# Optimization experiments

Measured on AMD Instinct MI355X. Metric: run time of the kernel, lower is better.

The kernel has to match this reference:

```python
import jax, jax.numpy as jnp
import numpy as np

DYN_CH = 16   # dyn_ch
MASK_CH = 16  # mask_ch (use_low_level_info=True -> num_bases=16)
UP_F = 8      # upsample_f
POUT = 256    # pad_out_channel


def _conv(x, w, padding):
    # NCHW conv, stride 1
    return jax.lax.conv_general_dilated(x, w, (1, 1), padding,
                                        dimension_numbers=('NCHW', 'OIHW', 'NCHW'))


def _bn(x, scale, shift):
    # inference-mode (Sync)BatchNorm folded to affine: scale=gamma/sqrt(var+eps), shift=beta-mean*scale
    return x * scale[None, :, None, None] + shift[None, :, None, None]


def _padconv(x, w, b, cin, cout, relu):
    # Faithful math of padconv(repeat -> mul -> grouped ones-conv -> bias -> relu),
    # expressed as a per-pixel dynamic 1x1 conv. Since w/b are nearest-upsampled
    # from HxW by factor f, we contract at low resolution per fxf block instead of
    # materializing the cout*cin-channel repeated tensors.
    # x: [B, cin, H*f, W*f]; w: [B, cout*cin, H, W]; b: [B, cout, H, W]
    B, _, Hf, Wf = x.shape
    H, W = w.shape[2], w.shape[3]
    f = Hf // H
    xb = x.reshape(B, cin, H, f, W, f)
    wr = w.reshape(B, cout, cin, H, W)
    out = jnp.einsum('bchpwq,bochw->bohpwq', xb, wr) + b[:, :, :, None, :, None]
    out = out.reshape(B, cout, Hf, Wf)
    return jax.nn.relu(out) if relu else out


def setup_inputs() -> dict:
    key = jax.random.key(0)
    ks = jax.random.split(key, 8)
    B, H, W = 8, 16, 16
    f = UP_F
    num_out = (2 + 16) * 16 + 16 + 16 * 16 + 16 + 16 * 256 + 256  # 4928
    inp = {}
    inp['res5'] = jax.random.normal(ks[0], (B, 2048, H, W), jnp.float32)
    inp['res2'] = jax.random.normal(ks[1], (B, 256, H * f, W * f), jnp.float32)
    inp['bottleneck_w'] = jax.random.normal(ks[2], (512, 2048, 3, 3), jnp.float32) * 0.01
    inp['bn1_scale'] = jnp.ones((512,), jnp.float32)
    inp['bn1_shift'] = jnp.zeros((512,), jnp.float32)
    inp['cls0_w'] = jax.random.normal(ks[3], (1024, 1024, 3, 3), jnp.float32) * 0.01
    inp['bn2_scale'] = jnp.ones((1024,), jnp.float32)
    inp['bn2_shift'] = jnp.zeros((1024,), jnp.float32)
    inp['cls1_w'] = jax.random.normal(ks[4], (num_out, 1024, 1, 1), jnp.float32) * 0.01
    inp['cls1_b'] = jnp.zeros((num_out,), jnp.float32)
    inp['c1a_w'] = jax.random.normal(ks[5], (48, 256, 3, 3), jnp.float32) * 0.02
    inp['bn3_scale'] = jnp.ones((48,), jnp.float32)
    inp['bn3_shift'] = jnp.zeros((48,), jnp.float32)
    inp['c1b_w'] = jax.random.normal(ks[6], (16, 48, 1, 1), jnp.float32) * 0.05
    inp['c1b_b'] = jnp.zeros((16,), jnp.float32)
    inp['cat_scale'] = jnp.ones((18,), jnp.float32)
    inp['cat_shift'] = jnp.zeros((18,), jnp.float32)
    return inp


def reference(res5, res2, bottleneck_w, bn1_scale, bn1_shift, cls0_w, bn2_scale,
              bn2_shift, cls1_w, cls1_b, c1a_w, bn3_scale, bn3_shift, c1b_w,
              c1b_b, cat_scale, cat_shift):
    B, _, H, W = res5.shape
    f = UP_F
    # bottleneck: conv3x3 -> BN -> relu
    x = jax.nn.relu(_bn(_conv(res5, bottleneck_w, 'SAME'), bn1_scale, bn1_shift))
    # global image pool, broadcast back, concat
    gp = jnp.broadcast_to(jnp.mean(x, axis=(2, 3), keepdims=True), x.shape)
    x = jnp.concatenate([x, gp], axis=1)
    # classifier: conv3x3 -> BN -> relu -> conv1x1 (+bias) => hyper-network params
    x = jax.nn.relu(_bn(_conv(x, cls0_w, 'SAME'), bn2_scale, bn2_shift))
    x = _conv(x, cls1_w, 'VALID') + cls1_b[None, :, None, None]  # [B, 4928, H, W]
    # c1_bottleneck on res2 (low-level features at H*f x W*f)
    c1 = jax.nn.relu(_bn(_conv(res2, c1a_w, 'SAME'), bn3_scale, bn3_shift))
    c1 = _conv(c1, c1b_w, 'VALID') + c1b_b[None, :, None, None]  # [B, 16, H*f, W*f]
    # split hyper-net output into per-pixel MLP weights/biases
    ch, nb = DYN_CH, MASK_CH
    sizes = [(2 + nb) * ch, ch, ch * ch, ch, ch * POUT, POUT]
    splits = np.cumsum(sizes)[:-1].tolist()
    w0, b0, w1, b1, w2, b2 = jnp.split(x, splits, axis=1)
    # coord grid: per fxf block, (x, y) in [0,1), tiled over HxW blocks
    xs = jnp.arange(f, dtype=jnp.float32) / f
    gy, gx = jnp.meshgrid(xs, xs, indexing='ij')
    loc = jnp.stack([gx, gy], axis=0)               # [2, f, f]
    coord = jnp.tile(loc, (1, H, W))                # [2, H*f, W*f]
    coord = jnp.broadcast_to(coord[None], (B, 2, H * f, W * f))
    inp = _bn(jnp.concatenate([coord, c1], axis=1), cat_scale, cat_shift)  # cat_norm
    # 3-layer per-pixel dynamic MLP (padconv trick, fused here)
    h = _padconv(inp, w0, b0, 2 + nb, ch, True)
    h = _padconv(h, w1, b1, ch, ch, True)
    out = _padconv(h, w2, b2, ch, POUT, False)      # [B, 256, H*f, W*f]
    return out
```

## Files before the change

### kernel.cpp

```cpp
#include <hip/hip_runtime.h>

#define B8 8

typedef __attribute__((ext_vector_type(8))) short short8;
typedef __attribute__((ext_vector_type(4))) float floatx4;

static __device__ __forceinline__ unsigned short f2bf(float f) {
  unsigned int u = __float_as_uint(f);
  unsigned int r = (u + 0x7fffu + ((u >> 16) & 1u)) >> 16;
  return (unsigned short)r;
}

__global__ __launch_bounds__(256) void wtransform(
    const float* __restrict__ w, unsigned short* __restrict__ wT,
    int Cout, int Cin)
{
  int idx = blockIdx.x * 256 + threadIdx.x;
  if (idx >= Cout * Cin) return;
  int ci = idx % Cin, co = idx / Cin;
  const float* s = w + (size_t)idx * 9;
#pragma unroll
  for (int t = 0; t < 9; ++t)
    wT[((size_t)t * Cout + co) * Cin + ci] = f2bf(s[t]);
}

__global__ __launch_bounds__(256) void cvt_bf16(
    const float* __restrict__ w, unsigned short* __restrict__ o, int n)
{
  int i = blockIdx.x * 256 + threadIdx.x;
  if (i < n) o[i] = f2bf(w[i]);
}

__global__ __launch_bounds__(256, 2) void conv3x3_mfma(
    const void* __restrict__ inv,
    const unsigned short* __restrict__ wT,
    float* __restrict__ part, int Cin, int Cout, int nCoBlk, int nSlice,
    int inBf16)
{
  int t = blockIdx.x;
  int slice = t % nSlice; t /= nSlice;
  int ph = t & 1; t >>= 1;
  int cb = t % nCoBlk; t /= nCoBlk;
  int b = t;
  int ciSlice = Cin / nSlice;
  int nTiles = ciSlice >> 5;

  __shared__ unsigned short sIn[10 * 18 * 40];

  int tid = threadIdx.x;
  int lane = tid & 63, wave = tid >> 6;
  int wc = wave >> 1, wp = wave & 1;
  int l15 = lane & 15, q = lane >> 4;

  for (int i = tid; i < (10 * 18 * 40) / 2; i += 256) ((unsigned int*)sIn)[i] = 0u;

  floatx4 acc[4][4];
#pragma unroll
  for (int ct = 0; ct < 4; ++ct)
#pragma unroll
    for (int pt = 0; pt < 4; ++pt) acc[ct][pt] = (floatx4){0.f, 0.f, 0.f, 0.f};

  int coBase = cb * 128 + wc * 64;
  int gr0 = ph * 7;
  int sr0 = 1 - ph;

  int gofs[18], lofs[18];
#pragma unroll
  for (int k = 0; k < 18; ++k) {
    int i = tid + k * 256;
    int px = i & 15, r9 = i >> 4;
    int rr = r9 % 9, ci = r9 / 9;
    gofs[k] = ci * 256 + (gr0 + rr) * 16 + px;
    lofs[k] = ((sr0 + rr) * 18 + 1 + px) * 40 + ci;
  }
  const float* inbF = (const float*)inv + (size_t)b * Cin * 256;
  const unsigned short* inbU = (const unsigned short*)inv + (size_t)b * Cin * 256;

  unsigned int pf[18];
  {
    int ci0 = slice * ciSlice;
    if (inBf16) {
#pragma unroll
      for (int k = 0; k < 18; ++k) pf[k] = inbU[(size_t)ci0 * 256 + gofs[k]];
    } else {
#pragma unroll
      for (int k = 0; k < 18; ++k)
        pf[k] = __float_as_uint(inbF[(size_t)ci0 * 256 + gofs[k]]);
    }
  }

  for (int ct2 = 0; ct2 < nTiles; ++ct2) {
    int ci0 = slice * ciSlice + ct2 * 32;
    __syncthreads();
    if (inBf16) {
#pragma unroll
      for (int k = 0; k < 18; ++k) sIn[lofs[k]] = (unsigned short)pf[k];
    } else {
#pragma unroll
      for (int k = 0; k < 18; ++k) sIn[lofs[k]] = f2bf(__uint_as_float(pf[k]));
    }
    __syncthreads();
    if (ct2 + 1 < nTiles) {
      int cin0 = ci0 + 32;
      if (inBf16) {
#pragma unroll
        for (int k = 0; k < 18; ++k) pf[k] = inbU[(size_t)cin0 * 256 + gofs[k]];
      } else {
#pragma unroll
        for (int k = 0; k < 18; ++k)
          pf[k] = __float_as_uint(inbF[(size_t)cin0 * 256 + gofs[k]]);
      }
    }
#pragma unroll
    for (int ky = 0; ky < 3; ++ky) {
#pragma unroll
      for (int kx = 0; kx < 3; ++kx) {
        int tap = ky * 3 + kx;
        const unsigned short* wbase =
            wT + ((size_t)(tap * Cout + coBase + l15)) * Cin + ci0 + q * 8;
        short8 af[4];
#pragma unroll
        for (int ct = 0; ct < 4; ++ct)
          af[ct] = *(const short8*)(wbase + (size_t)ct * 16 * Cin);
        short8 bf[4];
#pragma unroll
        for (int pt = 0; pt < 4; ++pt) {
          int sRow = wp * 4 + pt + ky;
          int sCol = l15 + kx;
          bf[pt] = *(const short8*)&sIn[(sRow * 18 + sCol) * 40 + q * 8];
        }
#pragma unroll
        for (int ct = 0; ct < 4; ++ct)
#pragma unroll
          for (int pt = 0; pt < 4; ++pt)
            acc[ct][pt] = __builtin_amdgcn_mfma_f32_16x16x32_bf16(
                af[ct], bf[pt], acc[ct][pt], 0, 0, 0);
      }
    }
  }

  float* po = part + ((size_t)(slice * B8 + b) * Cout) * 256;
#pragma unroll
  for (int ct = 0; ct < 4; ++ct) {
#pragma unroll
    for (int pt = 0; pt < 4; ++pt) {
      int co = coBase + ct * 16 + q * 4;
      int px = ph * 128 + wp * 64 + pt * 16 + l15;
#pragma unroll
      for (int r = 0; r < 4; ++r)
        po[(size_t)(co + r) * 256 + px] = acc[ct][pt][r];
    }
  }
}

__global__ __launch_bounds__(256) void combine1(
    const float* __restrict__ part, const float* __restrict__ scale,
    const float* __restrict__ shift, unsigned short* __restrict__ out,
    int Cout, int nSlice, int outStride)
{
  int c = blockIdx.x % Cout, b = blockIdx.x / Cout;
  int tid = threadIdx.x;
  float s = 0.0f;
  for (int sl = 0; sl < nSlice; ++sl)
    s += part[(((size_t)sl * B8 + b) * Cout + c) * 256 + tid];
  float v = fmaf(s, scale[c], shift[c]);
  v = v > 0.0f ? v : 0.0f;
  out[((size_t)b * outStride + c) * 256 + tid] = f2bf(v);
  __shared__ float red[4];
  float w = v;
#pragma unroll
  for (int off = 32; off > 0; off >>= 1) w += __shfl_down(w, off, 64);
  if ((tid & 63) == 0) red[tid >> 6] = w;
  __syncthreads();
  float m = (red[0] + red[1] + red[2] + red[3]) * (1.0f / 256.0f);
  out[((size_t)b * outStride + Cout + c) * 256 + tid] = f2bf(m);
}

__global__ __launch_bounds__(256) void combine2T(
    const float* __restrict__ part, const float* __restrict__ scale,
    const float* __restrict__ shift, unsigned short* __restrict__ x2T)
{
  int t = blockIdx.x;
  int cg = t & 3;
  int pxg = (t >> 2) & 15;
  int b = t >> 6;
  int c16 = threadIdx.x >> 4, px16 = threadIdx.x & 15;
  int px = pxg * 16 + px16;
#pragma unroll
  for (int k = 0; k < 4; ++k) {
    int cBase = cg * 256 + k * 64 + c16 * 4;
    unsigned short v4[4];
#pragma unroll
    for (int j = 0; j < 4; ++j) {
      int c = cBase + j;
      float s = 0.0f;
#pragma unroll
      for (int sl = 0; sl < 4; ++sl)
        s += part[(((size_t)sl * B8 + b) * 1024 + c) * 256 + px];
      float v = fmaf(s, scale[c], shift[c]);
      v4[j] = f2bf(v > 0.0f ? v : 0.0f);
    }
    *(ushort2*)&x2T[((size_t)b * 256 + px) * 1024 + cBase] =
        *(ushort2*)&v4[0];
    *(ushort2*)&x2T[((size_t)b * 256 + px) * 1024 + cBase + 2] =
        *(ushort2*)&v4[2];
  }
}

__global__ __launch_bounds__(256, 2) void hyper_gemm(
    const unsigned short* __restrict__ wH,
    const unsigned short* __restrict__ x2T,
    const float* __restrict__ bias,
    float* __restrict__ hyper)
{
  int cb = blockIdx.x % 77, b = blockIdx.x / 77;
  int tid = threadIdx.x;
  int lane = tid & 63, w = tid >> 6;
  int l15 = lane & 15, q = lane >> 4;

  floatx4 acc[4][4];
#pragma unroll
  for (int ct = 0; ct < 4; ++ct)
#pragma unroll
    for (int pt = 0; pt < 4; ++pt) acc[ct][pt] = (floatx4){0.f, 0.f, 0.f, 0.f};

  const unsigned short* wp0 = wH + ((size_t)(cb * 64 + l15)) * 1024 + q * 8;
  const unsigned short* xp0 =
      x2T + ((size_t)(b * 256 + w * 64 + l15)) * 1024 + q * 8;

  for (int ci0 = 0; ci0 < 1024; ci0 += 32) {
    short8 af[4], bf[4];
#pragma unroll
    for (int ct = 0; ct < 4; ++ct)
      af[ct] = *(const short8*)(wp0 + (size_t)ct * 16 * 1024 + ci0);
#pragma unroll
    for (int pt = 0; pt < 4; ++pt)
      bf[pt] = *(const short8*)(xp0 + (size_t)pt * 16 * 1024 + ci0);
#pragma unroll
    for (int ct = 0; ct < 4; ++ct)
#pragma unroll
      for (int pt = 0; pt < 4; ++pt)
        acc[ct][pt] = __builtin_amdgcn_mfma_f32_16x16x32_bf16(
            af[ct], bf[pt], acc[ct][pt], 0, 0, 0);
  }

#pragma unroll
  for (int ct = 0; ct < 4; ++ct) {
    int co = cb * 64 + ct * 16 + q * 4;
#pragma unroll
    for (int pt = 0; pt < 4; ++pt) {
      int px = w * 64 + pt * 16 + l15;
#pragma unroll
      for (int r = 0; r < 4; ++r)
        hyper[((size_t)b * 4928 + co + r) * 256 + px] = acc[ct][pt][r] + bias[co + r];
    }
  }
}

__global__ __launch_bounds__(256, 2) void conv3x3_hi_mfma(
    const float* __restrict__ in,
    const unsigned short* __restrict__ wT,
    const float* __restrict__ scale, const float* __restrict__ shift,
    float* __restrict__ out)
{
  int t = blockIdx.x;
  int tile = t & 63;
  int b = t >> 6;
  int ty0 = (tile >> 3) << 4, tx0 = (tile & 7) << 4;

  __shared__ unsigned short sIn[18 * 18 * 40];

  int tid = threadIdx.x;
  int lane = tid & 63, w = tid >> 6;
  int l15 = lane & 15, q = lane >> 4;

  int slotA = tid;
  int rowA = slotA / 18, colA = slotA % 18;
  int gyA = ty0 + rowA - 1, gxA = tx0 + colA - 1;
  bool vA = (unsigned)gyA < 128u && (unsigned)gxA < 128u;
  const float* gA = in + (size_t)b * 256 * 16384 + (vA ? (gyA * 128 + gxA) : 0);
  int slotB = 256 + tid;
  bool hasB = tid < 68;
  int rowB = slotB / 18, colB = slotB % 18;
  int gyB = ty0 + rowB - 1, gxB = tx0 + colB - 1;
  bool vB = hasB && (unsigned)gyB < 128u && (unsigned)gxB < 128u;
  const float* gB = in + (size_t)b * 256 * 16384 + (vB ? (gyB * 128 + gxB) : 0);

  floatx4 acc[3][4];
#pragma unroll
  for (int ct = 0; ct < 3; ++ct)
#pragma unroll
    for (int pt = 0; pt < 4; ++pt) acc[ct][pt] = (floatx4){0.f, 0.f, 0.f, 0.f};

  float pA[32], pB[32];
#pragma unroll
  for (int cp = 0; cp < 32; ++cp) pA[cp] = vA ? gA[(size_t)cp * 16384] : 0.0f;
  if (hasB) {
#pragma unroll
    for (int cp = 0; cp < 32; ++cp) pB[cp] = vB ? gB[(size_t)cp * 16384] : 0.0f;
  }

  for (int ci0 = 0; ci0 < 256; ci0 += 32) {
    __syncthreads();
    unsigned int* sU = (unsigned int*)sIn;
#pragma unroll
    for (int cp = 0; cp < 16; ++cp)
      sU[slotA * 20 + cp] =
          (unsigned)f2bf(pA[2 * cp]) | ((unsigned)f2bf(pA[2 * cp + 1]) << 16);
    if (hasB) {
#pragma unroll
      for (int cp = 0; cp < 16; ++cp)
        sU[slotB * 20 + cp] =
            (unsigned)f2bf(pB[2 * cp]) | ((unsigned)f2bf(pB[2 * cp + 1]) << 16);
    }
    __syncthreads();
    if (ci0 + 32 < 256) {
#pragma unroll
      for (int cp = 0; cp < 32; ++cp)
        pA[cp] = vA ? gA[(size_t)(ci0 + 32 + cp) * 16384] : 0.0f;
      if (hasB) {
#pragma unroll
        for (int cp = 0; cp < 32; ++cp)
          pB[cp] = vB ? gB[(size_t)(ci0 + 32 + cp) * 16384] : 0.0f;
      }
    }
#pragma unroll
    for (int ky = 0; ky < 3; ++ky) {
#pragma unroll
      for (int kx = 0; kx < 3; ++kx) {
        int tap = ky * 3 + kx;
        const unsigned short* wbase =
            wT + ((size_t)(tap * 48 + l15)) * 256 + ci0 + q * 8;
        short8 af[3];
#pragma unroll
        for (int ct = 0; ct < 3; ++ct)
          af[ct] = *(const short8*)(wbase + (size_t)ct * 16 * 256);
        short8 bf[4];
#pragma unroll
        for (int pt = 0; pt < 4; ++pt) {
          int sRow = w * 4 + pt + ky;
          int sCol = l15 + kx;
          bf[pt] = *(const short8*)&sIn[(sRow * 18 + sCol) * 40 + q * 8];
        }
#pragma unroll
        for (int ct = 0; ct < 3; ++ct)
#pragma unroll
          for (int pt = 0; pt < 4; ++pt)
            acc[ct][pt] = __builtin_amdgcn_mfma_f32_16x16x32_bf16(
                af[ct], bf[pt], acc[ct][pt], 0, 0, 0);
      }
    }
  }

#pragma unroll
  for (int ct = 0; ct < 3; ++ct) {
#pragma unroll
    for (int pt = 0; pt < 4; ++pt) {
      int oy = ty0 + w * 4 + pt, ox = tx0 + l15;
#pragma unroll
      for (int r = 0; r < 4; ++r) {
        int c = ct * 16 + q * 4 + r;
        float v = fmaf(acc[ct][pt][r], scale[c], shift[c]);
        v = v > 0.0f ? v : 0.0f;
        out[((size_t)b * 48 + c) * 16384 + oy * 128 + ox] = v;
      }
    }
  }
}

__global__ __launch_bounds__(256) void conv1x1_lo(
    const float* __restrict__ in, const float* __restrict__ wgt,
    const float* __restrict__ bias, float* __restrict__ out)
{
  int b = blockIdx.x >> 6;
  int px = ((blockIdx.x & 63) << 8) + threadIdx.x;
  float acc[16];
#pragma unroll
  for (int co = 0; co < 16; ++co) acc[co] = 0.0f;
#pragma unroll 4
  for (int ci = 0; ci < 48; ++ci) {
    float xv = in[((size_t)b * 48 + ci) * 16384 + px];
#pragma unroll
    for (int co = 0; co < 16; ++co) acc[co] = fmaf(xv, wgt[co * 48 + ci], acc[co]);
  }
#pragma unroll
  for (int co = 0; co < 16; ++co)
    out[((size_t)b * 16 + co) * 16384 + px] = acc[co] + bias[co];
}

__global__ __launch_bounds__(256) void dyn_mlp(
    const float* __restrict__ hyper, const float* __restrict__ c1,
    const float* __restrict__ catS, const float* __restrict__ catB,
    float* __restrict__ out)
{
  int t = blockIdx.x;
  int q = t & 3;
  int h = (t >> 2) & 15;
  int b = t >> 6;
  int tid = threadIdx.x;
  int xf = tid & 127, r2 = tid >> 7;
  int w = xf >> 3;

  __shared__ float smem[16 * 578];
  __shared__ float sB2[16 * 33];

  const float* hypb = hyper + (size_t)b * 4928 * 256 + h * 16;

  for (int i = tid; i < 576 * 16; i += 256) {
    int ch = i >> 4, ww = i & 15;
    smem[ww * 578 + ch] = hypb[(size_t)ch * 256 + ww];
  }

  float cs[18], cb[18];
#pragma unroll
  for (int i = 0; i < 18; ++i) { cs[i] = catS[i]; cb[i] = catB[i]; }

  float inpv[4][18];
  int yf0 = h * 8 + r2 * 4;
  float cx = (float)(xf & 7) * 0.125f;
#pragma unroll
  for (int k = 0; k < 4; ++k) {
    inpv[k][0] = fmaf(cx, cs[0], cb[0]);
    inpv[k][1] = fmaf((float)((yf0 + k) & 7) * 0.125f, cs[1], cb[1]);
#pragma unroll
    for (int ci = 0; ci < 16; ++ci) {
      float v = c1[((size_t)b * 16 + ci) * 16384 + (size_t)(yf0 + k) * 128 + xf];
      inpv[k][2 + ci] = fmaf(v, cs[2 + ci], cb[2 + ci]);
    }
  }
  __syncthreads();

  const float* sw = smem + w * 578;
  float h0v[4][16];
  {
    const float2* w0p = (const float2*)sw;
#pragma unroll
    for (int co = 0; co < 16; ++co) {
      float a0 = sw[288 + co], a1 = a0, a2 = a0, a3 = a0;
#pragma unroll
      for (int c2 = 0; c2 < 9; ++c2) {
        float2 wv = w0p[co * 9 + c2];
        a0 = fmaf(wv.x, inpv[0][2 * c2], a0); a0 = fmaf(wv.y, inpv[0][2 * c2 + 1], a0);
        a1 = fmaf(wv.x, inpv[1][2 * c2], a1); a1 = fmaf(wv.y, inpv[1][2 * c2 + 1], a1);
        a2 = fmaf(wv.x, inpv[2][2 * c2], a2); a2 = fmaf(wv.y, inpv[2][2 * c2 + 1], a2);
        a3 = fmaf(wv.x, inpv[3][2 * c2], a3); a3 = fmaf(wv.y, inpv[3][2 * c2 + 1], a3);
      }
      h0v[0][co] = fmaxf(a0, 0.0f); h0v[1][co] = fmaxf(a1, 0.0f);
      h0v[2][co] = fmaxf(a2, 0.0f); h0v[3][co] = fmaxf(a3, 0.0f);
    }
  }
  float h1v[4][16];
  {
    const float2* w1p = (const float2*)(sw + 304);
#pragma unroll
    for (int co = 0; co < 16; ++co) {
      float a0 = sw[560 + co], a1 = a0, a2 = a0, a3 = a0;
#pragma unroll
      for (int c2 = 0; c2 < 8; ++c2) {
        float2 wv = w1p[co * 8 + c2];
        a0 = fmaf(wv.x, h0v[0][2 * c2], a0); a0 = fmaf(wv.y, h0v[0][2 * c2 + 1], a0);
        a1 = fmaf(wv.x, h0v[1][2 * c2], a1); a1 = fmaf(wv.y, h0v[1][2 * c2 + 1], a1);
        a2 = fmaf(wv.x, h0v[2][2 * c2], a2); a2 = fmaf(wv.y, h0v[2][2 * c2 + 1], a2);
        a3 = fmaf(wv.x, h0v[3][2 * c2], a3); a3 = fmaf(wv.y, h0v[3][2 * c2 + 1], a3);
      }
      h1v[0][co] = fmaxf(a0, 0.0f); h1v[1][co] = fmaxf(a1, 0.0f);
      h1v[2][co] = fmaxf(a2, 0.0f); h1v[3][co] = fmaxf(a3, 0.0f);
    }
  }

  for (int chunk = 0; chunk < 2; ++chunk) {
    int po0 = q * 64 + chunk * 32;
    __syncthreads();
    for (int i = tid; i < 8192; i += 256) {
      int ch = i >> 4, ww = i & 15;
      smem[ww * 518 + ch] = hypb[(size_t)(576 + po0 * 16 + ch) * 256 + ww];
    }
    for (int i = tid; i < 512; i += 256) {
      int po = i >> 4, ww = i & 15;
      sB2[ww * 33 + po] = hypb[(size_t)(4672 + po0 + po) * 256 + ww];
    }
    __syncthreads();
    const float2* w2p = (const float2*)(smem + w * 518);
    const float* sb2 = sB2 + w * 33;
#pragma unroll 4
    for (int po = 0; po < 32; ++po) {
      float a0 = sb2[po], a1 = a0, a2 = a0, a3 = a0;
#pragma unroll
      for (int c2 = 0; c2 < 8; ++c2) {
        float2 wv = w2p[po * 8 + c2];
        a0 = fmaf(wv.x, h1v[0][2 * c2], a0); a0 = fmaf(wv.y, h1v[0][2 * c2 + 1], a0);
        a1 = fmaf(wv.x, h1v[1][2 * c2], a1); a1 = fmaf(wv.y, h1v[1][2 * c2 + 1], a1);
        a2 = fmaf(wv.x, h1v[2][2 * c2], a2); a2 = fmaf(wv.y, h1v[2][2 * c2 + 1], a2);
        a3 = fmaf(wv.x, h1v[3][2 * c2], a3); a3 = fmaf(wv.y, h1v[3][2 * c2 + 1], a3);
      }
      size_t ob = ((size_t)b * 256 + po0 + po) * 16384 + (size_t)yf0 * 128 + xf;
      out[ob] = a0; out[ob + 128] = a1; out[ob + 256] = a2; out[ob + 384] = a3;
    }
  }
}

extern "C" void kernel_launch(void* const* d_in, const int* in_sizes, int n_in,
                              void* d_out, int out_size, void* d_ws, size_t ws_size,
                              hipStream_t stream) {
  const float* res5 = (const float*)d_in[0];
  const float* res2 = (const float*)d_in[1];
  const float* bw   = (const float*)d_in[2];
  const float* bn1s = (const float*)d_in[3];
  const float* bn1b = (const float*)d_in[4];
  const float* c0w  = (const float*)d_in[5];
  const float* bn2s = (const float*)d_in[6];
  const float* bn2b = (const float*)d_in[7];
  const float* cls1w = (const float*)d_in[8];
  const float* cls1b = (const float*)d_in[9];
  const float* c1aw = (const float*)d_in[10];
  const float* bn3s = (const float*)d_in[11];
  const float* bn3b = (const float*)d_in[12];
  const float* c1bw = (const float*)d_in[13];
  const float* c1bb = (const float*)d_in[14];
  const float* catS = (const float*)d_in[15];
  const float* catB = (const float*)d_in[16];
  float* out = (float*)d_out;
  float* ws = (float*)d_ws;

  unsigned short* wT2u  = (unsigned short*)(ws);
  unsigned short* x2cat = (unsigned short*)(ws + 4718592);
  unsigned short* wT48  = (unsigned short*)(ws + 4718592);
  unsigned short* x2T   = (unsigned short*)(ws + 5767168);
  float* hyper          = ws + 6815744;
  unsigned short* wT1u  = (unsigned short*)(ws + 6815744);
  float* partial        = ws + 16908288;
  unsigned short* wH    = (unsigned short*)(ws + 16908288);
  float* c1mid          = ws + 16908288;
  float* c1             = ws + 23199744;

  wtransform<<<(512 * 2048 + 255) / 256, 256, 0, stream>>>(bw, wT1u, 512, 2048);
  wtransform<<<(1024 * 1024 + 255) / 256, 256, 0, stream>>>(c0w, wT2u, 1024, 1024);

  conv3x3_mfma<<<8 * 4 * 2 * 8, 256, 0, stream>>>(res5, wT1u, partial, 2048, 512, 4, 8, 0);
  combine1<<<8 * 512, 256, 0, stream>>>(partial, bn1s, bn1b, x2cat, 512, 8, 1024);
  conv3x3_mfma<<<8 * 8 * 2 * 4, 256, 0, stream>>>(x2cat, wT2u, partial, 1024, 1024, 8, 4, 1);
  combine2T<<<8 * 16 * 4, 256, 0, stream>>>(partial, bn2s, bn2b, x2T);
  cvt_bf16<<<(4928 * 1024 + 255) / 256, 256, 0, stream>>>(cls1w, wH, 4928 * 1024);
  hyper_gemm<<<77 * 8, 256, 0, stream>>>(wH, x2T, cls1b, hyper);
  wtransform<<<(48 * 256 + 255) / 256, 256, 0, stream>>>(c1aw, wT48, 48, 256);
  conv3x3_hi_mfma<<<8 * 64, 256, 0, stream>>>(res2, wT48, bn3s, bn3b, c1mid);
  conv1x1_lo<<<8 * 64, 256, 0, stream>>>(c1mid, c1bw, c1bb, c1);
  dyn_mlp<<<8 * 16 * 4, 256, 0, stream>>>(hyper, c1, catS, catB, out);
}
```

Measured before the change: 727.7 us.

## Pre-transpose res2 to NHWC bf16 and fuse 1x1 conv into high-res conv

New measurement: 760.8 us. 1.05x slower.

```diff
diff --git a/kernel.cpp b/kernel.cpp
--- a/kernel.cpp
+++ b/kernel.cpp
@@ -29,6 +29,165 @@
 {
   int i = blockIdx.x * 256 + threadIdx.x;
   if (i < n) o[i] = f2bf(w[i]);
+}
+
+__global__ __launch_bounds__(256) void nchw2nhwc_bf16(
+    const float* __restrict__ in, unsigned short* __restrict__ out)
+{
+  int t = blockIdx.x;
+  int pb = t & 63;
+  int cb = (t >> 6) & 7;
+  int b = t >> 9;
+
+  __shared__ unsigned short sT[32][260];
+
+  int tid = threadIdx.x;
+  int c4 = tid >> 6;
+  int px4 = (tid & 63) << 2;
+
+  const float* ip = in + ((size_t)(b * 256 + cb * 32) * 16384) + pb * 256;
+#pragma unroll
+  for (int cc = 0; cc < 8; ++cc) {
+    int ci = cc * 4 + c4;
+    float4 v = *(const float4*)&ip[(size_t)ci * 16384 + px4];
+    unsigned int p0 = (unsigned)f2bf(v.x) | ((unsigned)f2bf(v.y) << 16);
+    unsigned int p1 = (unsigned)f2bf(v.z) | ((unsigned)f2bf(v.w) << 16);
+    *(unsigned int*)&sT[ci][px4] = p0;
+    *(unsigned int*)&sT[ci][px4 + 2] = p1;
+  }
+  __syncthreads();
+
+  int px = tid;
+  unsigned short* op =
+      out + ((size_t)(b * 16384 + pb * 256 + px) * 256) + cb * 32;
+#pragma unroll
+  for (int j = 0; j < 4; ++j) {
+    short8 o;
+#pragma unroll
+    for (int k = 0; k < 8; ++k) o[k] = (short)sT[j * 8 + k][px];
+    *(short8*)&op[j * 8] = o;
+  }
+}
+
+__global__ __launch_bounds__(256, 2) void conv3x3_hi_nhwc(
+    const unsigned short* __restrict__ xh,
+    const unsigned short* __restrict__ wT,
+    const float* __restrict__ scale, const float* __restrict__ shift,
+    const float* __restrict__ w1,
+    const float* __restrict__ b1,
+    float* __restrict__ c1)
+{
+  int t = blockIdx.x;
+  int tile = t & 63;
+  int b = t >> 6;
+  int ty0 = (tile >> 3) << 4, tx0 = (tile & 7) << 4;
+
+  __shared__ float sW1[16 * 48];
+  __shared__ float sB1[16];
+
+  int tid = threadIdx.x;
+  for (int i = tid; i < 768; i += 256) sW1[i] = w1[i];
+  if (tid < 16) sB1[tid] = b1[tid];
+  __syncthreads();
+
+  int lane = tid & 63, w = tid >> 6;
+  int l15 = lane & 15, q = lane >> 4;
+
+  const unsigned short* xb = xh + (size_t)b * 16384 * 256 + q * 8;
+  int ofs[6][3];
+  bool vv[6][3];
+#pragma unroll
+  for (int rr = 0; rr < 6; ++rr) {
+    int gy = ty0 + w * 4 - 1 + rr;
+#pragma unroll
+    for (int cc = 0; cc < 3; ++cc) {
+      int gx = tx0 + l15 - 1 + cc;
+      bool v = (unsigned)gy < 128u && (unsigned)gx < 128u;
+      vv[rr][cc] = v;
+      ofs[rr][cc] = v ? ((gy * 128 + gx) * 256) : 0;
+    }
+  }
+
+  floatx4 acc[3][4];
+#pragma unroll
+  for (int ct = 0; ct < 3; ++ct)
+#pragma unroll
+    for (int pt = 0; pt < 4; ++pt) acc[ct][pt] = (floatx4){0.f, 0.f, 0.f, 0.f};
+
+  const short8 z8 = (short8){0, 0, 0, 0, 0, 0, 0, 0};
+
+  for (int ci0 = 0; ci0 < 256; ci0 += 32) {
+    short8 pix[6][3];
+#pragma unroll
+    for (int rr = 0; rr < 6; ++rr)
+#pragma unroll
+      for (int cc = 0; cc < 3; ++cc)
+        pix[rr][cc] =
+            vv[rr][cc] ? *(const short8*)&xb[ofs[rr][cc] + ci0] : z8;
+#pragma unroll
+    for (int ky = 0; ky < 3; ++ky) {
+#pragma unroll
+      for (int kx = 0; kx < 3; ++kx) {
+        int tap = ky * 3 + kx;
+        const unsigned short* wbase =
+            wT + ((size_t)(tap * 48 + l15)) * 256 + ci0 + q * 8;
+        short8 af[3];
+#pragma unroll
+        for (int ct = 0; ct < 3; ++ct)
+          af[ct] = *(const short8*)(wbase + ct * 16 * 256);
+#pragma unroll
+        for (int ct = 0; ct < 3; ++ct)
+#pragma unroll
+          for (int pt = 0; pt < 4; ++pt)
+            acc[ct][pt] = __builtin_amdgcn_mfma_f32_16x16x32_bf16(
+                af[ct], pix[pt + ky][kx], acc[ct][pt], 0, 0, 0);
+      }
+    }
+  }
+
+#pragma unroll
+  for (int ct = 0; ct < 3; ++ct) {
+#pragma unroll
+    for (int r = 0; r < 4; ++r) {
+      int c = ct * 16 + q * 4 + r;
+      float sc = scale[c], sh = shift[c];
+#pragma unroll
+      for (int pt = 0; pt < 4; ++pt) {
+        float x = fmaf(acc[ct][pt][r], sc, sh);
+        acc[ct][pt][r] = x > 0.0f ? x : 0.0f;
+      }
+    }
+  }
+
+  float* cp = c1 + (size_t)b * 16 * 16384 + (size_t)ty0 * 128 + tx0 + l15;
+#pragma unroll
+  for (int co = 0; co < 16; ++co) {
+    float wv[12];
+#pragma unroll
+    for (int ct = 0; ct < 3; ++ct)
+#pragma unroll
+      for (int r = 0; r < 4; ++r)
+        wv[ct * 4 + r] = sW1[co * 48 + ct * 16 + q * 4 + r];
+    float s[4];
+#pragma unroll
+    for (int pt = 0; pt < 4; ++pt) {
+      float a = 0.0f;
+#pragma unroll
+      for (int ct = 0; ct < 3; ++ct)
+#pragma unroll
+        for (int r = 0; r < 4; ++r)
+          a = fmaf(wv[ct * 4 + r], acc[ct][pt][r], a);
+      a += __shfl_xor(a, 16, 64);
+      a += __shfl_xor(a, 32, 64);
+      s[pt] = a;
+    }
+    if (q == (co >> 2)) {
+      float bb = sB1[co];
+#pragma unroll
+      for (int pt = 0; pt < 4; ++pt)
+        cp[(size_t)co * 16384 + (w * 4 + pt) * 128] = s[pt] + bb;
+    }
+  }
 }
 
 __global__ __launch_bounds__(256, 2) void conv3x3_mfma(
@@ -255,137 +414,6 @@
         hyper[((size_t)b * 4928 + co + r) * 256 + px] = acc[ct][pt][r] + bias[co + r];
     }
   }
-}
-
-__global__ __launch_bounds__(256, 2) void conv3x3_hi_mfma(
-    const float* __restrict__ in,
-    const unsigned short* __restrict__ wT,
-    const float* __restrict__ scale, const float* __restrict__ shift,
-    float* __restrict__ out)
-{
-  int t = blockIdx.x;
-  int tile = t & 63;
-  int b = t >> 6;
-  int ty0 = (tile >> 3) << 4, tx0 = (tile & 7) << 4;
-
-  __shared__ unsigned short sIn[18 * 18 * 40];
-
-  int tid = threadIdx.x;
-  int lane = tid & 63, w = tid >> 6;
-  int l15 = lane & 15, q = lane >> 4;
-
-  int slotA = tid;
-  int rowA = slotA / 18, colA = slotA % 18;
-  int gyA = ty0 + rowA - 1, gxA = tx0 + colA - 1;
-  bool vA = (unsigned)gyA < 128u && (unsigned)gxA < 128u;
-  const float* gA = in + (size_t)b * 256 * 16384 + (vA ? (gyA * 128 + gxA) : 0);
-  int slotB = 256 + tid;
-  bool hasB = tid < 68;
-  int rowB = slotB / 18, colB = slotB % 18;
-  int gyB = ty0 + rowB - 1, gxB = tx0 + colB - 1;
-  bool vB = hasB && (unsigned)gyB < 128u && (unsigned)gxB < 128u;
-  const float* gB = in + (size_t)b * 256 * 16384 + (vB ? (gyB * 128 + gxB) : 0);
-
-  floatx4 acc[3][4];
-#pragma unroll
-  for (int ct = 0; ct < 3; ++ct)
-#pragma unroll
-    for (int pt = 0; pt < 4; ++pt) acc[ct][pt] = (floatx4){0.f, 0.f, 0.f, 0.f};
-
-  float pA[32], pB[32];
-#pragma unroll
-  for (int cp = 0; cp < 32; ++cp) pA[cp] = vA ? gA[(size_t)cp * 16384] : 0.0f;
-  if (hasB) {
-#pragma unroll
-    for (int cp = 0; cp < 32; ++cp) pB[cp] = vB ? gB[(size_t)cp * 16384] : 0.0f;
-  }
-
-  for (int ci0 = 0; ci0 < 256; ci0 += 32) {
-    __syncthreads();
-    unsigned int* sU = (unsigned int*)sIn;
-#pragma unroll
-    for (int cp = 0; cp < 16; ++cp)
-      sU[slotA * 20 + cp] =
-          (unsigned)f2bf(pA[2 * cp]) | ((unsigned)f2bf(pA[2 * cp + 1]) << 16);
-    if (hasB) {
-#pragma unroll
-      for (int cp = 0; cp < 16; ++cp)
-        sU[slotB * 20 + cp] =
-            (unsigned)f2bf(pB[2 * cp]) | ((unsigned)f2bf(pB[2 * cp + 1]) << 16);
-    }
-    __syncthreads();
-    if (ci0 + 32 < 256) {
-#pragma unroll
-      for (int cp = 0; cp < 32; ++cp)
-        pA[cp] = vA ? gA[(size_t)(ci0 + 32 + cp) * 16384] : 0.0f;
-      if (hasB) {
-#pragma unroll
-        for (int cp = 0; cp < 32; ++cp)
-          pB[cp] = vB ? gB[(size_t)(ci0 + 32 + cp) * 16384] : 0.0f;
-      }
-    }
-#pragma unroll
-    for (int ky = 0; ky < 3; ++ky) {
-#pragma unroll
-      for (int kx = 0; kx < 3; ++kx) {
-        int tap = ky * 3 + kx;
-        const unsigned short* wbase =
-            wT + ((size_t)(tap * 48 + l15)) * 256 + ci0 + q * 8;
-        short8 af[3];
-#pragma unroll
-        for (int ct = 0; ct < 3; ++ct)
-          af[ct] = *(const short8*)(wbase + (size_t)ct * 16 * 256);
-        short8 bf[4];
-#pragma unroll
-        for (int pt = 0; pt < 4; ++pt) {
-          int sRow = w * 4 + pt + ky;
-          int sCol = l15 + kx;
-          bf[pt] = *(const short8*)&sIn[(sRow * 18 + sCol) * 40 + q * 8];
-        }
-#pragma unroll
-        for (int ct = 0; ct < 3; ++ct)
-#pragma unroll
-          for (int pt = 0; pt < 4; ++pt)
-            acc[ct][pt] = __builtin_amdgcn_mfma_f32_16x16x32_bf16(
-                af[ct], bf[pt], acc[ct][pt], 0, 0, 0);
-      }
-    }
-  }
-
-#pragma unroll
-  for (int ct = 0; ct < 3; ++ct) {
-#pragma unroll
-    for (int pt = 0; pt < 4; ++pt) {
-      int oy = ty0 + w * 4 + pt, ox = tx0 + l15;
-#pragma unroll
-      for (int r = 0; r < 4; ++r) {
-        int c = ct * 16 + q * 4 + r;
-        float v = fmaf(acc[ct][pt][r], scale[c], shift[c]);
-        v = v > 0.0f ? v : 0.0f;
-        out[((size_t)b * 48 + c) * 16384 + oy * 128 + ox] = v;
-      }
-    }
-  }
-}
-
-__global__ __launch_bounds__(256) void conv1x1_lo(
-    const float* __restrict__ in, const float* __restrict__ wgt,
-    const float* __restrict__ bias, float* __restrict__ out)
-{
-  int b = blockIdx.x >> 6;
-  int px = ((blockIdx.x & 63) << 8) + threadIdx.x;
-  float acc[16];
-#pragma unroll
-  for (int co = 0; co < 16; ++co) acc[co] = 0.0f;
-#pragma unroll 4
-  for (int ci = 0; ci < 48; ++ci) {
-    float xv = in[((size_t)b * 48 + ci) * 16384 + px];
-#pragma unroll
-    for (int co = 0; co < 16; ++co) acc[co] = fmaf(xv, wgt[co * 48 + ci], acc[co]);
-  }
-#pragma unroll
-  for (int co = 0; co < 16; ++co)
-    out[((size_t)b * 16 + co) * 16384 + px] = acc[co] + bias[co];
 }
 
 __global__ __launch_bounds__(256) void dyn_mlp(
@@ -523,27 +551,33 @@
   float* ws = (float*)d_ws;
 
   unsigned short* wT2u  = (unsigned short*)(ws);
+  float* c1             = ws;
+  unsigned short* wT48  = (unsigned short*)(ws + 2097152);
   unsigned short* x2cat = (unsigned short*)(ws + 4718592);
-  unsigned short* wT48  = (unsigned short*)(ws + 4718592);
   unsigned short* x2T   = (unsigned short*)(ws + 5767168);
   float* hyper          = ws + 6815744;
   unsigned short* wT1u  = (unsigned short*)(ws + 6815744);
   float* partial        = ws + 16908288;
   unsigned short* wH    = (unsigned short*)(ws + 16908288);
-  float* c1mid          = ws + 16908288;
-  float* c1             = ws + 23199744;
+  unsigned short* x2nhwc = (unsigned short*)(ws + 16908288);
 
   wtransform<<<(512 * 2048 + 255) / 256, 256, 0, stream>>>(bw, wT1u, 512, 2048);
   wtransform<<<(1024 * 1024 + 255) / 256, 256, 0, stream>>>(c0w, wT2u, 1024, 1024);
-
   conv3x3_mfma<<<8 * 4 * 2 * 8, 256, 0, stream>>>(res5, wT1u, partial, 2048, 512, 4, 8, 0);
   combine1<<<8 * 512, 256, 0, stream>>>(partial, bn1s, bn1b, x2cat, 512, 8, 1024);
   conv3x3_mfma<<<8 * 8 * 2 * 4, 256, 0, stream>>>(x2cat, wT2u, partial, 1024, 1024, 8, 4, 1);
   combine2T<<<8 * 16 * 4, 256, 0, stream>>>(partial, bn2s, bn2b, x2T);
   cvt_bf16<<<(4928 * 1024 + 255) / 256, 256, 0, stream>>>(cls1w, wH, 4928 * 1024);
   hyper_gemm<<<77 * 8, 256, 0, stream>>>(wH, x2T, cls1b, hyper);
+
   wtransform<<<(48 * 256 + 255) / 256, 256, 0, stream>>>(c1aw, wT48, 48, 256);
-  conv3x3_hi_mfma<<<8 * 64, 256, 0, stream>>>(res2, wT48, bn3s, bn3b, c1mid);
-  conv1x1_lo<<<8 * 64, 256, 0, stream>>>(c1mid, c1bw, c1bb, c1);
+  for (int half = 0; half < 2; ++half) {
+    nchw2nhwc_bf16<<<4 * 8 * 64, 256, 0, stream>>>(
+        res2 + (size_t)half * 4 * 256 * 16384, x2nhwc);
+    conv3x3_hi_nhwc<<<4 * 64, 256, 0, stream>>>(
+        x2nhwc, wT48, bn3s, bn3b, c1bw, c1bb,
+        c1 + (size_t)half * 4 * 16 * 16384);
+  }
+
   dyn_mlp<<<8 * 16 * 4, 256, 0, stream>>>(hyper, c1, catS, catB, out);
 }
```
